# Optimization experiments

Hardware: AMD Instinct MI355X
Metric: run time of the kernel (lower is better)

The kernel has to match this reference:

```python
import jax, jax.numpy as jnp
import numpy as np

NEG_SLOPE = 0.2
EPS = 1e-16  # PyG softmax denominator epsilon

N_NODES = 50000
N_EDGES = 800000
IN_CH = 128
HID = 64
HEADS = 4


def setup_inputs() -> dict:
    key = jax.random.key(0)
    ks = jax.random.split(key, 10)
    rng = np.random.default_rng(0)
    src = rng.integers(0, N_NODES, N_EDGES)
    dst = rng.integers(0, N_NODES, N_EDGES)
    dst = np.where(src == dst, (dst + 1) % N_NODES, dst)  # no pre-existing self-loops
    edge_index = jnp.asarray(np.stack([src, dst]), dtype=jnp.int32)
    s = 0.1
    return {
        "x": jax.random.normal(ks[0], (N_NODES, IN_CH), jnp.float32),
        "edge_index": edge_index,
        "W1": jax.random.normal(ks[1], (IN_CH, HEADS * HID), jnp.float32) * s,
        "att_src1": jax.random.normal(ks[2], (HEADS, HID), jnp.float32) * s,
        "att_dst1": jax.random.normal(ks[3], (HEADS, HID), jnp.float32) * s,
        "b1": jnp.zeros((HEADS * HID,), jnp.float32),
        "W2": jax.random.normal(ks[4], (HEADS * HID, HID), jnp.float32) * s,
        "att_src2": jax.random.normal(ks[5], (1, HID), jnp.float32) * s,
        "att_dst2": jax.random.normal(ks[6], (1, HID), jnp.float32) * s,
        "b2": jnp.zeros((HID,), jnp.float32),
    }


def _gat_conv(x, src, dst, W, att_src, att_dst, bias, heads, out_ch, concat):
    """PyG GATConv: messages flow src -> dst, softmax over edges sharing dst."""
    n = x.shape[0]
    h = (x @ W).reshape(n, heads, out_ch)                  # [N,H,C]
    a_s = jnp.einsum('nhc,hc->nh', h, att_src)             # [N,H]
    a_d = jnp.einsum('nhc,hc->nh', h, att_dst)             # [N,H]
    e = jax.nn.leaky_relu(a_s[src] + a_d[dst], NEG_SLOPE)  # [E,H]
    e_max = jax.ops.segment_max(e, dst, num_segments=n)
    e_max = jnp.where(jnp.isfinite(e_max), e_max, 0.0)
    ex = jnp.exp(e - e_max[dst])                           # [E,H]
    denom = jax.ops.segment_sum(ex, dst, num_segments=n)   # [N,H]
    alpha = ex / (denom[dst] + EPS)                        # [E,H]
    msg = h[src] * alpha[:, :, None]                       # [E,H,C]
    out = jax.ops.segment_sum(msg, dst, num_segments=n)    # [N,H,C]
    if concat:
        out = out.reshape(n, heads * out_ch)
    else:
        out = out.mean(axis=1)
    return out + bias


def reference(x, edge_index, W1, att_src1, att_dst1, b1, W2, att_src2, att_dst2, b2):
    n = x.shape[0]
    loops = jnp.arange(n, dtype=edge_index.dtype)
    src = jnp.concatenate([edge_index[0], loops])  # GATConv add_self_loops=True
    dst = jnp.concatenate([edge_index[1], loops])
    h = _gat_conv(x, src, dst, W1, att_src1, att_dst1, b1, HEADS, HID, True)
    h = jax.nn.elu(h)
    h = _gat_conv(h, src, dst, W2, att_src2, att_dst2, b2, 1, HID, False)
    node_u = h[edge_index[0]]
    node_v = h[edge_index[1]]
    return jnp.concatenate([node_u, node_v], axis=-1)  # [E, 2*HID]
```

## Files before the change

### kernel.cpp

```cpp
#include <hip/hip_runtime.h>
#include <hip/hip_bf16.h>

#define NEG_SLOPE 0.2f
#define EPS 1e-16f

typedef short  bf16x8  __attribute__((ext_vector_type(8)));
typedef float  f32x4   __attribute__((ext_vector_type(4)));
typedef float  nfloat4 __attribute__((ext_vector_type(4)));

__device__ __forceinline__ float bf2f(unsigned short u) {
    union { unsigned int i; float f; } c; c.i = ((unsigned int)u) << 16; return c.f;
}
__device__ __forceinline__ ushort f2bf(float f) {
    __hip_bfloat16 b = __float2bfloat16(f);
    return *(ushort*)&b;
}

__global__ void hist_k(const int* __restrict__ dst, int E, int* __restrict__ deg) {
    int e = blockIdx.x * blockDim.x + threadIdx.x;
    if (e < E) atomicAdd(&deg[dst[e]], 1);
}

__global__ __launch_bounds__(1024) void scan1_k(const int* __restrict__ deg, int* __restrict__ offs,
                                                int* __restrict__ bsum, int n) {
    __shared__ int tmp[1024];
    int t = threadIdx.x;
    int i = blockIdx.x * 1024 + t;
    int v = (i < n) ? deg[i] : 0;
    tmp[t] = v;
    __syncthreads();
    int run = v;
    for (int off = 1; off < 1024; off <<= 1) {
        int add = (t >= off) ? tmp[t - off] : 0;
        __syncthreads();
        run += add;
        tmp[t] = run;
        __syncthreads();
    }
    if (i < n) offs[i] = run - v;
    if (t == 1023) bsum[blockIdx.x] = run;
}

__global__ void scan2_k(int* bsum, int nb) {
    if (blockIdx.x == 0 && threadIdx.x == 0) {
        int acc = 0;
        for (int i = 0; i < nb; i++) { int v = bsum[i]; bsum[i] = acc; acc += v; }
    }
}

__global__ __launch_bounds__(1024) void scan3_k(int* __restrict__ offs, const int* __restrict__ bsum,
                                                int n, int total) {
    int i = blockIdx.x * 1024 + threadIdx.x;
    if (i < n) offs[i] += bsum[blockIdx.x];
    if (i == 0) offs[n] = total;
}

__global__ void fill_k(const int* __restrict__ src, const int* __restrict__ dst, int E,
                       const int* __restrict__ offs, int* __restrict__ cur, int* __restrict__ csr) {
    int e = blockIdx.x * blockDim.x + threadIdx.x;
    if (e >= E) return;
    int d = dst[e];
    int pos = offs[d] + atomicAdd(&cur[d], 1);
    csr[pos] = src[e];
}

__global__ void wprep_k(const float* __restrict__ W1, const float* __restrict__ aS1,
                        const float* __restrict__ aD1, const float* __restrict__ W2,
                        const float* __restrict__ aS2, const float* __restrict__ aD2,
                        ushort* __restrict__ b1hi, ushort* __restrict__ b1lo,
                        ushort* __restrict__ b2hi, ushort* __restrict__ b2lo) {
    int tid = blockIdx.x * blockDim.x + threadIdx.x;
    const int N1 = 17 * 4 * 64 * 8;
    const int N2 = 5 * 8 * 64 * 8;
    if (tid < N1) {
        int j = tid & 7, lane = (tid >> 3) & 63, ks = (tid >> 9) & 3, nt = tid >> 11;
        int k = ks * 32 + (lane >> 4) * 8 + j;
        int col = nt * 16 + (lane & 15);
        float v = 0.f;
        if (col < 256) v = W1[k * 256 + col];
        else if (col < 264) {
            int cc = col - 256, h = cc & 3;
            const float* att = (cc < 4) ? aS1 : aD1;
            float s = 0.f;
            for (int c = 0; c < 64; c++) s += W1[k * 256 + h * 64 + c] * att[h * 64 + c];
            v = s;
        }
        ushort hi = f2bf(v);
        int idx = ((nt * 4 + ks) * 64 + lane) * 8 + j;
        b1hi[idx] = hi; b1lo[idx] = f2bf(v - bf2f(hi));
    } else if (tid < N1 + N2) {
        int t2 = tid - N1;
        int j = t2 & 7, lane = (t2 >> 3) & 63, ks = (t2 >> 9) & 7, nt = t2 >> 12;
        int k = ks * 32 + (lane >> 4) * 8 + j;
        int col = nt * 16 + (lane & 15);
        float v = 0.f;
        if (col < 64) v = W2[k * 64 + col];
        else if (col == 64) { float s = 0.f; for (int c = 0; c < 64; c++) s += W2[k * 64 + c] * aS2[c]; v = s; }
        else if (col == 65) { float s = 0.f; for (int c = 0; c < 64; c++) s += W2[k * 64 + c] * aD2[c]; v = s; }
        ushort hi = f2bf(v);
        int idx = ((nt * 8 + ks) * 64 + lane) * 8 + j;
        b2hi[idx] = hi; b2lo[idx] = f2bf(v - bf2f(hi));
    }
}

__global__ __launch_bounds__(256) void gemm1_mfma_k(const float* __restrict__ x,
                                                    const bf16x8* __restrict__ bhi, const bf16x8* __restrict__ blo,
                                                    ushort* __restrict__ h1b, float* __restrict__ as1,
                                                    float* __restrict__ ad1, int N) {
    __shared__ ushort hs[4][16][256];
    int wid = threadIdx.x >> 6, lane = threadIdx.x & 63;
    int m0 = (blockIdx.x * 4 + wid) * 16;
    if (m0 >= N) return;
    int row = lane & 15, grp = lane >> 4;
    int rr = (m0 + row < N) ? (m0 + row) : (N - 1);
    const float4* xrow = (const float4*)(x + (size_t)rr * 128);

    bf16x8 ah[4], al[4];
#pragma unroll
    for (int ks = 0; ks < 4; ks++) {
        float4 f0 = xrow[ks * 8 + grp * 2];
        float4 f1 = xrow[ks * 8 + grp * 2 + 1];
        float fv[8] = {f0.x, f0.y, f0.z, f0.w, f1.x, f1.y, f1.z, f1.w};
#pragma unroll
        for (int j = 0; j < 8; j++) {
            ushort hi = f2bf(fv[j]);
            ah[ks][j] = (short)hi;
            al[ks][j] = (short)f2bf(fv[j] - bf2f(hi));
        }
    }

    int rows = N - m0; if (rows > 16) rows = 16;
    for (int nt = 0; nt < 17; nt++) {
        f32x4 acc = {0.f, 0.f, 0.f, 0.f};
#pragma unroll
        for (int ks = 0; ks < 4; ks++) {
            bf16x8 bh = bhi[(nt * 4 + ks) * 64 + lane];
            bf16x8 bl = blo[(nt * 4 + ks) * 64 + lane];
            acc = __builtin_amdgcn_mfma_f32_16x16x32_bf16(ah[ks], bh, acc, 0, 0, 0);
            acc = __builtin_amdgcn_mfma_f32_16x16x32_bf16(al[ks], bh, acc, 0, 0, 0);
            acc = __builtin_amdgcn_mfma_f32_16x16x32_bf16(ah[ks], bl, acc, 0, 0, 0);
        }
        if (nt < 16) {
            int col = nt * 16 + row, head = col >> 6, c = col & 63;
#pragma unroll
            for (int r = 0; r < 4; r++) hs[wid][grp * 4 + r][c * 4 + head] = f2bf(acc[r]);
        } else if (row < 8) {
#pragma unroll
            for (int r = 0; r < 4; r++) {
                int node = m0 + grp * 4 + r;
                if (node < N) {
                    if (row < 4) as1[node * 4 + row] = acc[r];
                    else         ad1[node * 4 + (row - 4)] = acc[r];
                }
            }
        }
    }
    ushort4* dst = (ushort4*)h1b + (size_t)m0 * 64;
    const ushort4* s4 = (const ushort4*)&hs[wid][0][0];
    for (int i = lane; i < rows * 64; i += 64) dst[i] = s4[i];
}

__global__ __launch_bounds__(256) void gemm2_mfma_k(const ushort* __restrict__ h1e,
                                                    const bf16x8* __restrict__ bhi, const bf16x8* __restrict__ blo,
                                                    ushort* __restrict__ h2b, float* __restrict__ as2,
                                                    float* __restrict__ ad2, int N) {
    __shared__ ushort hs[4][16][64];
    int wid = threadIdx.x >> 6, lane = threadIdx.x & 63;
    int m0 = (blockIdx.x * 4 + wid) * 16;
    if (m0 >= N) return;
    int row = lane & 15, grp = lane >> 4;
    const bf16x8* a8 = (const bf16x8*)h1e;
    bf16x8 a[8];
    int rr = (m0 + row < N) ? (m0 + row) : (N - 1);
    size_t rb = (size_t)rr * 32 + grp;
#pragma unroll
    for (int ks = 0; ks < 8; ks++) a[ks] = a8[rb + ks * 4];

    int rows = N - m0; if (rows > 16) rows = 16;
    for (int nt = 0; nt < 5; nt++) {
        f32x4 acc = {0.f, 0.f, 0.f, 0.f};
#pragma unroll
        for (int ks = 0; ks < 8; ks++) {
            bf16x8 bh = bhi[(nt * 8 + ks) * 64 + lane];
            bf16x8 bl = blo[(nt * 8 + ks) * 64 + lane];
            acc = __builtin_amdgcn_mfma_f32_16x16x32_bf16(a[ks], bh, acc, 0, 0, 0);
            acc = __builtin_amdgcn_mfma_f32_16x16x32_bf16(a[ks], bl, acc, 0, 0, 0);
        }
        if (nt < 4) {
            int col = nt * 16 + row;
#pragma unroll
            for (int r = 0; r < 4; r++) hs[wid][grp * 4 + r][col] = f2bf(acc[r]);
        } else if (row < 2) {
#pragma unroll
            for (int r = 0; r < 4; r++) {
                int node = m0 + grp * 4 + r;
                if (node < N) {
                    if (row == 0) as2[node] = acc[r];
                    else          ad2[node] = acc[r];
                }
            }
        }
    }
    ushort4* dst = (ushort4*)h2b + (size_t)m0 * 16;
    const ushort4* s4 = (const ushort4*)&hs[wid][0][0];
    for (int i = lane; i < rows * 16; i += 64) dst[i] = s4[i];
}

__global__ __launch_bounds__(256) void agg4_k(const ushort4* __restrict__ hb, const float4* __restrict__ asv,
                                              const float4* __restrict__ adv, const int* __restrict__ offs,
                                              const int* __restrict__ csr, const float* __restrict__ bias,
                                              ushort* __restrict__ out, int N) {
    int node = (int)(((size_t)blockIdx.x * blockDim.x + threadIdx.x) >> 6);
    int lane = threadIdx.x & 63;
    if (node >= N) return;
    int beg = offs[node], end = offs[node + 1];
    int total = end - beg + 1;
    float4 ad = adv[node];

    float den0 = 0.f, den1 = 0.f, den2 = 0.f, den3 = 0.f;
    float acc0 = 0.f, acc1 = 0.f, acc2 = 0.f, acc3 = 0.f;

    for (int base = 0; base < total; base += 64) {
        int i = base + lane;
        bool valid = i < total;
        int s = node;
        if (valid && i > 0) s = csr[beg + i - 1];
        float4 av = asv[s];
        float e0 = av.x + ad.x; e0 = e0 > 0.f ? e0 : NEG_SLOPE * e0;
        float e1 = av.y + ad.y; e1 = e1 > 0.f ? e1 : NEG_SLOPE * e1;
        float e2 = av.z + ad.z; e2 = e2 > 0.f ? e2 : NEG_SLOPE * e2;
        float e3 = av.w + ad.w; e3 = e3 > 0.f ? e3 : NEG_SLOPE * e3;
        float p0 = valid ? __expf(e0) : 0.f;
        float p1 = valid ? __expf(e1) : 0.f;
        float p2 = valid ? __expf(e2) : 0.f;
        float p3 = valid ? __expf(e3) : 0.f;
        float q0 = p0, q1 = p1, q2 = p2, q3 = p3;
#pragma unroll
        for (int off = 32; off >= 1; off >>= 1) {
            q0 += __shfl_xor(q0, off);
            q1 += __shfl_xor(q1, off);
            q2 += __shfl_xor(q2, off);
            q3 += __shfl_xor(q3, off);
        }
        den0 += q0; den1 += q1; den2 += q2; den3 += q3;

        int cn = total - base; if (cn > 64) cn = 64;
        int cn4 = (cn + 3) & ~3;
        for (int j = 0; j < cn4; j += 4) {
            int s0 = __shfl(s, j), s1 = __shfl(s, j + 1), s2 = __shfl(s, j + 2), s3 = __shfl(s, j + 3);
            ushort4 v0 = hb[(size_t)s0 * 64 + lane];
            ushort4 v1 = hb[(size_t)s1 * 64 + lane];
            ushort4 v2 = hb[(size_t)s2 * 64 + lane];
            ushort4 v3 = hb[(size_t)s3 * 64 + lane];
            float w00 = __shfl(p0, j), w01 = __shfl(p1, j), w02 = __shfl(p2, j), w03 = __shfl(p3, j);
            acc0 = fmaf(bf2f(v0.x), w00, acc0);
            acc1 = fmaf(bf2f(v0.y), w01, acc1);
            acc2 = fmaf(bf2f(v0.z), w02, acc2);
            acc3 = fmaf(bf2f(v0.w), w03, acc3);
            float w10 = __shfl(p0, j + 1), w11 = __shfl(p1, j + 1), w12 = __shfl(p2, j + 1), w13 = __shfl(p3, j + 1);
            acc0 = fmaf(bf2f(v1.x), w10, acc0);
            acc1 = fmaf(bf2f(v1.y), w11, acc1);
            acc2 = fmaf(bf2f(v1.z), w12, acc2);
            acc3 = fmaf(bf2f(v1.w), w13, acc3);
            float w20 = __shfl(p0, j + 2), w21 = __shfl(p1, j + 2), w22 = __shfl(p2, j + 2), w23 = __shfl(p3, j + 2);
            acc0 = fmaf(bf2f(v2.x), w20, acc0);
            acc1 = fmaf(bf2f(v2.y), w21, acc1);
            acc2 = fmaf(bf2f(v2.z), w22, acc2);
            acc3 = fmaf(bf2f(v2.w), w23, acc3);
            float w30 = __shfl(p0, j + 3), w31 = __shfl(p1, j + 3), w32 = __shfl(p2, j + 3), w33 = __shfl(p3, j + 3);
            acc0 = fmaf(bf2f(v3.x), w30, acc0);
            acc1 = fmaf(bf2f(v3.y), w31, acc1);
            acc2 = fmaf(bf2f(v3.z), w32, acc2);
            acc3 = fmaf(bf2f(v3.w), w33, acc3);
        }
    }

    ushort* op = out + (size_t)node * 256 + lane;
    float o;
    o = acc0 / (den0 + EPS) + bias[lane];        o = o > 0.f ? o : expm1f(o); op[0]   = f2bf(o);
    o = acc1 / (den1 + EPS) + bias[64 + lane];   o = o > 0.f ? o : expm1f(o); op[64]  = f2bf(o);
    o = acc2 / (den2 + EPS) + bias[128 + lane];  o = o > 0.f ? o : expm1f(o); op[128] = f2bf(o);
    o = acc3 / (den3 + EPS) + bias[192 + lane];  o = o > 0.f ? o : expm1f(o); op[192] = f2bf(o);
}

__global__ __launch_bounds__(256) void agg1_k(const ushort* __restrict__ h2b, const float* __restrict__ asv,
                                              const float* __restrict__ adv, const int* __restrict__ offs,
                                              const int* __restrict__ csr, const float* __restrict__ bias,
                                              float* __restrict__ out, int N) {
    int node = (int)(((size_t)blockIdx.x * blockDim.x + threadIdx.x) >> 6);
    int lane = threadIdx.x & 63;
    if (node >= N) return;
    int beg = offs[node], end = offs[node + 1];
    int total = end - beg + 1;
    float ad = adv[node];

    float den = 0.f, acc = 0.f;
    for (int base = 0; base < total; base += 64) {
        int i = base + lane;
        bool valid = i < total;
        int s = node;
        if (valid && i > 0) s = csr[beg + i - 1];
        float e = asv[s] + ad;
        e = e > 0.f ? e : NEG_SLOPE * e;
        float p = valid ? __expf(e) : 0.f;
        float q = p;
#pragma unroll
        for (int off = 32; off >= 1; off >>= 1) q += __shfl_xor(q, off);
        den += q;

        int cn = total - base; if (cn > 64) cn = 64;
        int cn4 = (cn + 3) & ~3;
        for (int j = 0; j < cn4; j += 4) {
            int s0 = __shfl(s, j), s1 = __shfl(s, j + 1), s2 = __shfl(s, j + 2), s3 = __shfl(s, j + 3);
            float h0 = bf2f(h2b[(size_t)s0 * 64 + lane]);
            float h1 = bf2f(h2b[(size_t)s1 * 64 + lane]);
            float h2v = bf2f(h2b[(size_t)s2 * 64 + lane]);
            float h3 = bf2f(h2b[(size_t)s3 * 64 + lane]);
            acc = fmaf(h0, __shfl(p, j), acc);
            acc = fmaf(h1, __shfl(p, j + 1), acc);
            acc = fmaf(h2v, __shfl(p, j + 2), acc);
            acc = fmaf(h3, __shfl(p, j + 3), acc);
        }
    }
    out[(size_t)node * 64 + lane] = acc / (den + EPS) + bias[lane];
}

__global__ void gather_k(const nfloat4* __restrict__ h2a4, const int* __restrict__ srcv,
                         const int* __restrict__ dstv, nfloat4* __restrict__ out, int E) {
    int t = blockIdx.x * blockDim.x + threadIdx.x;
    if (t >= E * 32) return;
    int e = t >> 5, q = t & 31;
    int node = (q < 16) ? srcv[e] : dstv[e];
    nfloat4 v = h2a4[(size_t)node * 16 + (q & 15)];
    __builtin_nontemporal_store(v, &out[t]);
}

extern "C" void kernel_launch(void* const* d_in, const int* in_sizes, int n_in,
                              void* d_out, int out_size, void* d_ws, size_t ws_size,
                              hipStream_t stream) {
    const float* x   = (const float*)d_in[0];
    const int*   ei  = (const int*)d_in[1];
    const float* W1  = (const float*)d_in[2];
    const float* aS1 = (const float*)d_in[3];
    const float* aD1 = (const float*)d_in[4];
    const float* b1  = (const float*)d_in[5];
    const float* W2  = (const float*)d_in[6];
    const float* aS2 = (const float*)d_in[7];
    const float* aD2 = (const float*)d_in[8];
    const float* b2  = (const float*)d_in[9];
    float* out = (float*)d_out;

    int N = in_sizes[0] / 128;
    int E = in_sizes[1] / 2;
    const int* srcv = ei;
    const int* dstv = ei + E;

    size_t off = 0;
    char* base = (char*)d_ws;
    auto alloc = [&](size_t bytes) -> void* {
        void* p = base + off;
        off = (off + bytes + 255) & ~(size_t)255;
        return p;
    };
    int*    deg  = (int*)alloc((size_t)2 * N * 4);
    int*    cur  = deg + N;
    int*    offs = (int*)alloc((size_t)(N + 1) * 4);
    int*    bsum = (int*)alloc(256 * 4);
    int*    csr  = (int*)alloc((size_t)E * 4);
    float*  as1  = (float*)alloc((size_t)N * 16);
    float*  ad1  = (float*)alloc((size_t)N * 16);
    float*  as2  = (float*)alloc((size_t)N * 4);
    float*  ad2  = (float*)alloc((size_t)N * 4);
    ushort* b1hi = (ushort*)alloc(17 * 4 * 64 * 8 * 2);
    ushort* b1lo = (ushort*)alloc(17 * 4 * 64 * 8 * 2);
    ushort* b2hi = (ushort*)alloc(5 * 8 * 64 * 8 * 2);
    ushort* b2lo = (ushort*)alloc(5 * 8 * 64 * 8 * 2);
    ushort* h1b  = (ushort*)alloc((size_t)N * 256 * 2);
    ushort* h1e  = (ushort*)alloc((size_t)N * 256 * 2);
    ushort* h2b  = h1b;
    float*  h2a  = (float*)(h1b + (size_t)N * 64);

    (void)hipMemsetAsync(deg, 0, (size_t)2 * N * 4, stream);

    int nbE = (E + 255) / 256;
    hist_k<<<nbE, 256, 0, stream>>>(dstv, E, deg);
    int nbS = (N + 1023) / 1024;
    scan1_k<<<nbS, 1024, 0, stream>>>(deg, offs, bsum, N);
    scan2_k<<<1, 64, 0, stream>>>(bsum, nbS);
    scan3_k<<<nbS, 1024, 0, stream>>>(offs, bsum, N, E);
    fill_k<<<nbE, 256, 0, stream>>>(srcv, dstv, E, offs, cur, csr);

    wprep_k<<<(17 * 4 * 64 * 8 + 5 * 8 * 64 * 8 + 255) / 256, 256, 0, stream>>>(
        W1, aS1, aD1, W2, aS2, aD2, b1hi, b1lo, b2hi, b2lo);

    int nstrip = (N + 15) / 16;
    int nbG1 = (nstrip + 3) / 4;
    gemm1_mfma_k<<<nbG1, 256, 0, stream>>>(x, (const bf16x8*)b1hi, (const bf16x8*)b1lo,
                                           h1b, as1, ad1, N);

    int nbA = (N * 64 + 255) / 256;
    agg4_k<<<nbA, 256, 0, stream>>>((const ushort4*)h1b, (const float4*)as1, (const float4*)ad1,
                                    offs, csr, b1, h1e, N);

    gemm2_mfma_k<<<nbG1, 256, 0, stream>>>(h1e, (const bf16x8*)b2hi, (const bf16x8*)b2lo,
                                           h2b, as2, ad2, N);

    agg1_k<<<nbA, 256, 0, stream>>>(h2b, as2, ad2, offs, csr, b2, h2a, N);

    int nbGth = (E * 32 + 255) / 256;
    gather_k<<<nbGth, 256, 0, stream>>>((const nfloat4*)h2a, srcv, dstv, (nfloat4*)out, E);
}
```

Measured before the change: 351.3 us.

## Fold scan2 into scan3, merge fill with wprep, store final features as bf16

Drops the single-thread scan2 kernel by having each scan3 block reduce the preceding block sums with a wave shuffle. Merges the CSR fill and weight-prep kernels into one launch split by block index. Stores layer-2 output as bf16 so the final edge gather reads half the bytes, at the cost of bf16 rounding on the output values.

```diff
diff --git a/kernel.cpp b/kernel.cpp
--- a/kernel.cpp
+++ b/kernel.cpp
@@ -41,38 +41,37 @@
     if (t == 1023) bsum[blockIdx.x] = run;
 }
 
-__global__ void scan2_k(int* bsum, int nb) {
-    if (blockIdx.x == 0 && threadIdx.x == 0) {
-        int acc = 0;
-        for (int i = 0; i < nb; i++) { int v = bsum[i]; bsum[i] = acc; acc += v; }
-    }
-}
-
 __global__ __launch_bounds__(1024) void scan3_k(int* __restrict__ offs, const int* __restrict__ bsum,
-                                                int n, int total) {
+                                                int n, int nb, int total) {
+    int lane = threadIdx.x & 63;
+    int v = (lane < nb && lane < (int)blockIdx.x) ? bsum[lane] : 0;
+#pragma unroll
+    for (int off = 32; off >= 1; off >>= 1) v += __shfl_xor(v, off);
     int i = blockIdx.x * 1024 + threadIdx.x;
-    if (i < n) offs[i] += bsum[blockIdx.x];
+    if (i < n) offs[i] += v;
     if (i == 0) offs[n] = total;
 }
 
-__global__ void fill_k(const int* __restrict__ src, const int* __restrict__ dst, int E,
-                       const int* __restrict__ offs, int* __restrict__ cur, int* __restrict__ csr) {
-    int e = blockIdx.x * blockDim.x + threadIdx.x;
-    if (e >= E) return;
-    int d = dst[e];
-    int pos = offs[d] + atomicAdd(&cur[d], 1);
-    csr[pos] = src[e];
-}
-
-__global__ void wprep_k(const float* __restrict__ W1, const float* __restrict__ aS1,
-                        const float* __restrict__ aD1, const float* __restrict__ W2,
-                        const float* __restrict__ aS2, const float* __restrict__ aD2,
-                        ushort* __restrict__ b1hi, ushort* __restrict__ b1lo,
-                        ushort* __restrict__ b2hi, ushort* __restrict__ b2lo) {
-    int tid = blockIdx.x * blockDim.x + threadIdx.x;
-    const int N1 = 17 * 4 * 64 * 8;
-    const int N2 = 5 * 8 * 64 * 8;
-    if (tid < N1) {
+#define NB_W1 (17 * 4 * 64 * 8)
+#define NB_W2 (5 * 8 * 64 * 8)
+__global__ void fill_wprep_k(const int* __restrict__ src, const int* __restrict__ dst, int E,
+                             const int* __restrict__ offs, int* __restrict__ cur, int* __restrict__ csr,
+                             int nbE,
+                             const float* __restrict__ W1, const float* __restrict__ aS1,
+                             const float* __restrict__ aD1, const float* __restrict__ W2,
+                             const float* __restrict__ aS2, const float* __restrict__ aD2,
+                             ushort* __restrict__ b1hi, ushort* __restrict__ b1lo,
+                             ushort* __restrict__ b2hi, ushort* __restrict__ b2lo) {
+    if ((int)blockIdx.x < nbE) {
+        int e = blockIdx.x * blockDim.x + threadIdx.x;
+        if (e >= E) return;
+        int d = dst[e];
+        int pos = offs[d] + atomicAdd(&cur[d], 1);
+        csr[pos] = src[e];
+        return;
+    }
+    int tid = (blockIdx.x - nbE) * blockDim.x + threadIdx.x;
+    if (tid < NB_W1) {
         int j = tid & 7, lane = (tid >> 3) & 63, ks = (tid >> 9) & 3, nt = tid >> 11;
         int k = ks * 32 + (lane >> 4) * 8 + j;
         int col = nt * 16 + (lane & 15);
@@ -88,8 +87,8 @@
         ushort hi = f2bf(v);
         int idx = ((nt * 4 + ks) * 64 + lane) * 8 + j;
         b1hi[idx] = hi; b1lo[idx] = f2bf(v - bf2f(hi));
-    } else if (tid < N1 + N2) {
-        int t2 = tid - N1;
+    } else if (tid < NB_W1 + NB_W2) {
+        int t2 = tid - NB_W1;
         int j = t2 & 7, lane = (t2 >> 3) & 63, ks = (t2 >> 9) & 7, nt = t2 >> 12;
         int k = ks * 32 + (lane >> 4) * 8 + j;
         int col = nt * 16 + (lane & 15);
@@ -286,7 +285,7 @@
 __global__ __launch_bounds__(256) void agg1_k(const ushort* __restrict__ h2b, const float* __restrict__ asv,
                                               const float* __restrict__ adv, const int* __restrict__ offs,
                                               const int* __restrict__ csr, const float* __restrict__ bias,
-                                              float* __restrict__ out, int N) {
+                                              ushort* __restrict__ out, int N) {
     int node = (int)(((size_t)blockIdx.x * blockDim.x + threadIdx.x) >> 6);
     int lane = threadIdx.x & 63;
     if (node >= N) return;
@@ -322,17 +321,18 @@
             acc = fmaf(h3, __shfl(p, j + 3), acc);
         }
     }
-    out[(size_t)node * 64 + lane] = acc / (den + EPS) + bias[lane];
-}
-
-__global__ void gather_k(const nfloat4* __restrict__ h2a4, const int* __restrict__ srcv,
+    out[(size_t)node * 64 + lane] = f2bf(acc / (den + EPS) + bias[lane]);
+}
+
+__global__ void gather_k(const ushort4* __restrict__ h2a16, const int* __restrict__ srcv,
                          const int* __restrict__ dstv, nfloat4* __restrict__ out, int E) {
     int t = blockIdx.x * blockDim.x + threadIdx.x;
     if (t >= E * 32) return;
     int e = t >> 5, q = t & 31;
     int node = (q < 16) ? srcv[e] : dstv[e];
-    nfloat4 v = h2a4[(size_t)node * 16 + (q & 15)];
-    __builtin_nontemporal_store(v, &out[t]);
+    ushort4 v = h2a16[(size_t)node * 16 + (q & 15)];
+    nfloat4 f = {bf2f(v.x), bf2f(v.y), bf2f(v.z), bf2f(v.w)};
+    __builtin_nontemporal_store(f, &out[t]);
 }
 
 extern "C" void kernel_launch(void* const* d_in, const int* in_sizes, int n_in,
@@ -371,14 +371,14 @@
     float*  ad1  = (float*)alloc((size_t)N * 16);
     float*  as2  = (float*)alloc((size_t)N * 4);
     float*  ad2  = (float*)alloc((size_t)N * 4);
-    ushort* b1hi = (ushort*)alloc(17 * 4 * 64 * 8 * 2);
-    ushort* b1lo = (ushort*)alloc(17 * 4 * 64 * 8 * 2);
-    ushort* b2hi = (ushort*)alloc(5 * 8 * 64 * 8 * 2);
-    ushort* b2lo = (ushort*)alloc(5 * 8 * 64 * 8 * 2);
+    ushort* b1hi = (ushort*)alloc(NB_W1 * 2);
+    ushort* b1lo = (ushort*)alloc(NB_W1 * 2);
+    ushort* b2hi = (ushort*)alloc(NB_W2 * 2);
+    ushort* b2lo = (ushort*)alloc(NB_W2 * 2);
     ushort* h1b  = (ushort*)alloc((size_t)N * 256 * 2);
     ushort* h1e  = (ushort*)alloc((size_t)N * 256 * 2);
     ushort* h2b  = h1b;
-    float*  h2a  = (float*)(h1b + (size_t)N * 64);
+    ushort* h2a  = h1b + (size_t)N * 64;
 
     (void)hipMemsetAsync(deg, 0, (size_t)2 * N * 4, stream);
 
@@ -386,12 +386,12 @@
     hist_k<<<nbE, 256, 0, stream>>>(dstv, E, deg);
     int nbS = (N + 1023) / 1024;
     scan1_k<<<nbS, 1024, 0, stream>>>(deg, offs, bsum, N);
-    scan2_k<<<1, 64, 0, stream>>>(bsum, nbS);
-    scan3_k<<<nbS, 1024, 0, stream>>>(offs, bsum, N, E);
-    fill_k<<<nbE, 256, 0, stream>>>(srcv, dstv, E, offs, cur, csr);
-
-    wprep_k<<<(17 * 4 * 64 * 8 + 5 * 8 * 64 * 8 + 255) / 256, 256, 0, stream>>>(
-        W1, aS1, aD1, W2, aS2, aD2, b1hi, b1lo, b2hi, b2lo);
+    scan3_k<<<nbS, 1024, 0, stream>>>(offs, bsum, N, nbS, E);
+
+    int nbW = (NB_W1 + NB_W2 + 255) / 256;
+    fill_wprep_k<<<nbE + nbW, 256, 0, stream>>>(srcv, dstv, E, offs, cur, csr, nbE,
+                                                W1, aS1, aD1, W2, aS2, aD2,
+                                                b1hi, b1lo, b2hi, b2lo);
 
     int nstrip = (N + 15) / 16;
     int nbG1 = (nstrip + 3) / 4;
@@ -408,5 +408,5 @@
     agg1_k<<<nbA, 256, 0, stream>>>(h2b, as2, ad2, offs, csr, b2, h2a, N);
 
     int nbGth = (E * 32 + 255) / 256;
-    gather_k<<<nbGth, 256, 0, stream>>>((const nfloat4*)h2a, srcv, dstv, (nfloat4*)out, E);
-}
+    gather_k<<<nbGth, 256, 0, stream>>>((const ushort4*)h2a, srcv, dstv, (nfloat4*)out, E);
+}
```

After: 312.3 us, median of 2. -11.1%, faster.
